# Optimization experiments

Hardware: AMD Instinct MI355X
Metric: run time of the kernel (lower is better)

The kernel has to match this reference:

```python
import jax, jax.numpy as jnp
import numpy as np

B, S, D_IN, M, H, F, L, D_OUT = 4, 1024, 256, 1024, 16, 8, 2, 256
HD = M // H
EPS = 1e-5


def setup_inputs() -> dict:
    key = jax.random.key(0)
    ks = iter(jax.random.split(key, 40))
    w = lambda *s: 0.02 * jax.random.normal(next(ks), s, dtype=jnp.float32)
    inp = {
        "x": jax.random.normal(next(ks), (B, S, D_IN), dtype=jnp.float32),
        # phase embedding params
        "Wemb": w(D_IN, M), "bemb": w(M),
        "Wamp": w(M, F), "bamp": w(F),
        "freqs": jnp.logspace(-1, 2, F, dtype=jnp.float32),
        "phase_off": w(F),
        # per-layer attention params, stacked on leading L axis
        "Wq": w(L, M, M), "bq": w(L, M),
        "Wk": w(L, M, M), "bk": w(L, M),
        "Wv": w(L, M, M), "bv": w(L, M),
        "Wo": w(L, M, M), "bo": w(L, M),
        "pbias": w(L, H, F),
        "ln_g": jnp.ones((L, M), dtype=jnp.float32),
        "ln_b": jnp.zeros((L, M), dtype=jnp.float32),
        # output projection MLP
        "W1": w(M, M // 2), "b1": w(M // 2),
        "W2": w(M // 2, D_OUT), "b2": w(D_OUT),
    }
    return inp


def _forward(x, Wemb, bemb, Wamp, bamp, freqs, phase_off,
             Wq, bq, Wk, bk, Wv, bv, Wo, bo, pbias, ln_g, ln_b,
             W1, b1, W2, b2):
    Bsz, Seq, _ = x.shape
    # --- TemporalPhaseEmbedding ---
    m = x @ Wemb + bemb                                   # [B,S,M]
    tc = jnp.arange(Seq, dtype=x.dtype) / Seq * (2.0 * jnp.pi)  # [S]
    amp = jax.nn.softmax(m @ Wamp + bamp, axis=-1)        # [B,S,F]
    pc = tc[:, None] * freqs[None, :] + phase_off         # [S,F] (batch-identical)
    # |m[...,None] * amp * e^{i*pc}| averaged over F == |m| * mean_F(amp)
    pf = jnp.abs(m) * jnp.mean(amp, axis=-1, keepdims=True)  # [B,S,M]
    # phase-coherence, batch-independent since pc is shared across batch
    coh = jnp.cos(pc[:, None, :] - pc[None, :, :])        # [S,S,F]
    scale = 1.0 / jnp.sqrt(jnp.asarray(HD, dtype=x.dtype))
    for l in range(L):
        res = pf
        Q = (pf @ Wq[l] + bq[l]).reshape(Bsz, Seq, H, HD)
        K = (pf @ Wk[l] + bk[l]).reshape(Bsz, Seq, H, HD)
        V = (pf @ Wv[l] + bv[l]).reshape(Bsz, Seq, H, HD)
        bias = jnp.einsum('stf,hf->hst', coh, pbias[l])   # [H,S,S]
        scores = jnp.einsum('bshd,bthd->bhst', Q, K) * scale + bias[None]
        w_attn = jax.nn.softmax(scores, axis=-1)
        att = jnp.einsum('bhst,bthd->bshd', w_attn, V).reshape(Bsz, Seq, M)
        att = att @ Wo[l] + bo[l]
        y = att + res
        mu = jnp.mean(y, axis=-1, keepdims=True)
        var = jnp.var(y, axis=-1, keepdims=True)
        pf = (y - mu) / jnp.sqrt(var + EPS) * ln_g[l] + ln_b[l]
    hdn = jax.nn.relu(pf @ W1 + b1)
    return hdn @ W2 + b2                                  # [B,S,D_OUT]


def reference(x, Wemb, bemb, Wamp, bamp, freqs, phase_off,
              Wq, bq, Wk, bk, Wv, bv, Wo, bo, pbias, ln_g, ln_b,
              W1, b1, W2, b2):
    return _forward(x, Wemb, bemb, Wamp, bamp, freqs, phase_off,
                    Wq, bq, Wk, bk, Wv, bv, Wo, bo, pbias, ln_g, ln_b,
                    W1, b1, W2, b2)
```

## Files before the change

kernel.cpp:

```cpp
#include <hip/hip_runtime.h>
#include <cmath>

#define B_    4
#define S_    1024
#define DIN_  256
#define M_    1024
#define H_    16
#define F_    8
#define L_    2
#define DOUT_ 256
#define NT_   4096

typedef unsigned short u16;
typedef unsigned int   u32;
typedef __bf16 bf16x8 __attribute__((ext_vector_type(8)));
typedef float  f32x4  __attribute__((ext_vector_type(4)));

#define LOG2E 1.4426950408889634f
#define QSCALE (0.125f * LOG2E)

__device__ __forceinline__ u16 f2b(float f) {
    u32 u = __builtin_bit_cast(u32, f);
    u += 0x7fffu + ((u >> 16) & 1u);
    return (u16)(u >> 16);
}
__device__ __forceinline__ float b2f(u32 h) {
    return __builtin_bit_cast(float, h << 16);
}
__device__ __forceinline__ void gload_lds16(const void* g, void* l) {
    __builtin_amdgcn_global_load_lds(
        (const __attribute__((address_space(1))) u32*)g,
        (__attribute__((address_space(3))) u32*)l, 16, 0, 0);
}

__global__ void qcsb_k(const float* __restrict__ freqs,
                       const float* __restrict__ poff,
                       const float* __restrict__ pb,
                       u16* __restrict__ qcs, u16* __restrict__ csb)
{
    const int QN = L_ * H_ * S_ * 16;
    int idx = blockIdx.x * 256 + threadIdx.x;
    if (idx < QN) {
        int f2 = idx & 15, f = f2 & 7;
        int s = (idx >> 4) & 1023;
        int lh = idx >> 14;
        float pc = ((float)s * (6.283185307179586f / 1024.f)) * freqs[f] + poff[f];
        float v = (f2 < 8) ? cosf(pc) : sinf(pc);
        qcs[idx] = f2b(pb[lh * 8 + f] * v * LOG2E);
    } else if (idx < QN + S_ * 16) {
        int i2 = idx - QN;
        int f2 = i2 & 15, f = f2 & 7;
        int s = i2 >> 4;
        float pc = ((float)s * (6.283185307179586f / 1024.f)) * freqs[f] + poff[f];
        csb[i2] = f2b((f2 < 8) ? cosf(pc) : sinf(pc));
    }
}

__global__ void bcat_k(const float* __restrict__ bq, const float* __restrict__ bk,
                       const float* __restrict__ bv, float* __restrict__ bqkv)
{
    int idx = blockIdx.x * 256 + threadIdx.x;
    int l = idx >= 3072;
    int j = idx - l * 3072;
    float v = (j < 1024) ? bq[l * 1024 + j]
            : (j < 2048) ? bk[l * 1024 + j - 1024]
                         : bv[l * 1024 + j - 2048];
    bqkv[idx] = v;
}

__global__ __launch_bounds__(256) void cvt_k(const float* __restrict__ src,
                                             u16* __restrict__ dst)
{
    int i = (blockIdx.x * 256 + threadIdx.x) * 4;
    float4 v = *(const float4*)(src + i);
    *(ushort4*)(dst + i) = make_ushort4(f2b(v.x), f2b(v.y), f2b(v.z), f2b(v.w));
}

__global__ __launch_bounds__(256) void cvtT_k(const float* __restrict__ src,
                                              u16* __restrict__ dst, int K, int N)
{
    __shared__ float t[32][33];
    src += (size_t)blockIdx.z * K * N;
    dst += (size_t)blockIdx.z * K * N;
    const int n0 = blockIdx.x * 32, k0 = blockIdx.y * 32;
    const int r = threadIdx.x >> 3, c4 = (threadIdx.x & 7) << 2;
    float4 v = *(const float4*)(src + (size_t)(k0 + r) * N + n0 + c4);
    t[r][c4 + 0] = v.x; t[r][c4 + 1] = v.y; t[r][c4 + 2] = v.z; t[r][c4 + 3] = v.w;
    __syncthreads();
    ushort4 o = make_ushort4(f2b(t[c4 + 0][r]), f2b(t[c4 + 1][r]),
                             f2b(t[c4 + 2][r]), f2b(t[c4 + 3][r]));
    *(ushort4*)(dst + (size_t)(n0 + r) * K + k0 + c4) = o;
}

__global__ __launch_bounds__(256) void cvtT3_k(const float* __restrict__ Wq,
                                               const float* __restrict__ Wk,
                                               const float* __restrict__ Wv,
                                               u16* __restrict__ dst)
{
    __shared__ float t[32][33];
    const int z = blockIdx.z, l = z / 3, which = z - l * 3;
    const float* src = (which == 0 ? Wq : which == 1 ? Wk : Wv) + (size_t)l * M_ * M_;
    u16* d = dst + (size_t)l * 3072 * 1024 + (size_t)which * 1024 * 1024;
    const int n0 = blockIdx.x * 32, k0 = blockIdx.y * 32;
    const int r = threadIdx.x >> 3, c4 = (threadIdx.x & 7) << 2;
    float4 v = *(const float4*)(src + (size_t)(k0 + r) * 1024 + n0 + c4);
    t[r][c4 + 0] = v.x; t[r][c4 + 1] = v.y; t[r][c4 + 2] = v.z; t[r][c4 + 3] = v.w;
    __syncthreads();
    ushort4 o = make_ushort4(f2b(t[c4 + 0][r]), f2b(t[c4 + 1][r]),
                             f2b(t[c4 + 2][r]), f2b(t[c4 + 3][r]));
    *(ushort4*)(d + (size_t)(n0 + r) * 1024 + k0 + c4) = o;
}

template<int EPI, int OUTBF>
__global__ __launch_bounds__(256, 2) void mgemm_k(
    const u16* __restrict__ A, const u16* __restrict__ Wt,
    const float* __restrict__ bias, void* __restrict__ Cout,
    u16* __restrict__ vt, int N, int K)
{
    __shared__ __attribute__((aligned(16))) u16 As[128 * 64];
    __shared__ __attribute__((aligned(16))) u16 Bs[128 * 64];
    const int tid = threadIdx.x;
    const int lane = tid & 63;
    const int bn = blockIdx.x, bm = blockIdx.y;
    const int wid = tid >> 6, wr = wid >> 1, wc = wid & 1;

    f32x4 acc[4][4];
#pragma unroll
    for (int m = 0; m < 4; ++m)
#pragma unroll
        for (int n = 0; n < 4; ++n) {
            f32x4 z = {0.f, 0.f, 0.f, 0.f};
            acc[m][n] = z;
        }

    const int r = lane & 15, g = lane >> 4;
    const int nk = K >> 6;

    for (int kt = 0; kt < nk; ++kt) {
        const int k0 = kt << 6;
        __syncthreads();
#pragma unroll
        for (int i = 0; i < 4; ++i) {
            int slot = i * 256 + tid;
            int row = slot >> 3;
            int kg = (slot & 7) ^ (row & 7);
            gload_lds16(A + (size_t)(bm * 128 + row) * K + k0 + kg * 8,
                        As + (size_t)(slot & ~63) * 8);
        }
#pragma unroll
        for (int i = 0; i < 4; ++i) {
            int slot = i * 256 + tid;
            int row = slot >> 3;
            int kg = (slot & 7) ^ (row & 7);
            gload_lds16(Wt + (size_t)(bn * 128 + row) * K + k0 + kg * 8,
                        Bs + (size_t)(slot & ~63) * 8);
        }
        __syncthreads();

#pragma unroll
        for (int ks = 0; ks < 2; ++ks) {
            bf16x8 af[4], bfr[4];
#pragma unroll
            for (int m = 0; m < 4; ++m) {
                int row = wr * 64 + m * 16 + r;
                int kg = (ks * 4 + g) ^ (row & 7);
                af[m] = *(const bf16x8*)(As + row * 64 + kg * 8);
            }
#pragma unroll
            for (int n = 0; n < 4; ++n) {
                int row = wc * 64 + n * 16 + r;
                int kg = (ks * 4 + g) ^ (row & 7);
                bfr[n] = *(const bf16x8*)(Bs + row * 64 + kg * 8);
            }
#pragma unroll
            for (int m = 0; m < 4; ++m)
#pragma unroll
                for (int n = 0; n < 4; ++n)
                    acc[m][n] = __builtin_amdgcn_mfma_f32_16x16x32_bf16(
                        af[m], bfr[n], acc[m][n], 0, 0, 0);
        }
    }

#pragma unroll
    for (int n = 0; n < 4; ++n) {
        const int gcol = bn * 128 + wc * 64 + n * 16 + r;
        const float bb = bias[gcol];
#pragma unroll
        for (int m = 0; m < 4; ++m) {
            const int grow0 = bm * 128 + wr * 64 + m * 16 + g * 4;
            if (EPI == 5 && gcol >= 2048) {
                int d = gcol - 2048;
                int bh = (grow0 >> 10) * 16 + (d >> 6);
                u16 pk[4];
#pragma unroll
                for (int q = 0; q < 4; ++q) pk[q] = f2b(acc[m][n][q] + bb);
                uint2 pv;
                pv.x = (u32)pk[0] | ((u32)pk[1] << 16);
                pv.y = (u32)pk[2] | ((u32)pk[3] << 16);
                *(uint2*)(vt + ((size_t)bh * 64 + (d & 63)) * 1024 + (grow0 & 1023)) = pv;
            } else {
#pragma unroll
                for (int q = 0; q < 4; ++q) {
                    float c = acc[m][n][q] + bb;
                    if (EPI == 1) c = fabsf(c) * 0.125f;
                    if (EPI == 2) c = fmaxf(c, 0.f);
                    if (EPI == 5) c = (gcol < 1024) ? c * QSCALE : c;
                    if (OUTBF)
                        ((u16*)Cout)[(size_t)(grow0 + q) * N + gcol] = f2b(c);
                    else
                        ((float*)Cout)[(size_t)(grow0 + q) * N + gcol] = c;
                }
            }
        }
    }
}

__global__ __launch_bounds__(512) void fattn_k(
    const u16* __restrict__ QKV, const u16* __restrict__ Vtg,
    const u16* __restrict__ csb, const u16* __restrict__ qcs,
    u16* __restrict__ Og)
{
    __shared__ __attribute__((aligned(16))) u16 Ks2[2][64 * 64];
    __shared__ __attribute__((aligned(16))) u16 Vt2[2][64 * 64];
    __shared__ __attribute__((aligned(16))) u16 Ext[2][64 * 16];
    __shared__ __attribute__((aligned(16))) u16 Pl[8][16 * 68];
    const int tid = threadIdx.x, lane = tid & 63, w = tid >> 6;
    const int c = lane & 15, g = lane >> 4;
    const int h = blockIdx.y, b = blockIdx.z, bh = b * 16 + h;
    const int s0 = blockIdx.x * 128;

    const uint4 zz = {0u, 0u, 0u, 0u};
    const bf16x8 zfrag = __builtin_bit_cast(bf16x8, zz);

    bf16x8 aq[3];
    {
        int sl = s0 + w * 16 + c;
        size_t tok = (size_t)b * 1024 + sl;
        aq[0] = *(const bf16x8*)(QKV + tok * 3072 + h * 64 + g * 8);
        aq[1] = *(const bf16x8*)(QKV + tok * 3072 + h * 64 + 32 + g * 8);
        aq[2] = (g < 2) ? *(const bf16x8*)(qcs + ((size_t)h * 1024 + sl) * 16 + g * 8)
                        : zfrag;
    }

    f32x4 oacc[4];
#pragma unroll
    for (int n = 0; n < 4; ++n) {
        f32x4 z = {0.f, 0.f, 0.f, 0.f};
        oacc[n] = z;
    }
    float lsum = 0.f;

    auto STAGE = [&](int buf, int t0) {
        int row = tid >> 3, gi = tid & 7;
        int kg = (gi ^ (row & 7)) * 8;
        gload_lds16(QKV + (size_t)(b * 1024 + t0 + row) * 3072 + 1024 + h * 64 + kg,
                    &Ks2[buf][(size_t)(tid & ~63) * 8]);
        gload_lds16(Vtg + (size_t)(bh * 64 + row) * 1024 + t0 + kg,
                    &Vt2[buf][(size_t)(tid & ~63) * 8]);
        if (tid < 128) {
            int r2 = tid >> 1, g2 = tid & 1;
            gload_lds16(csb + (size_t)(t0 + r2) * 16 + g2 * 8,
                        &Ext[buf][(size_t)(tid & ~63) * 8]);
        }
    };

    STAGE(0, 0);
    __builtin_amdgcn_sched_barrier(0);

    for (int it = 0; it < 16; ++it) {
        const int cur = it & 1;
        if (it < 15) {
            STAGE(cur ^ 1, (it + 1) << 6);
            if (w < 2) asm volatile("s_waitcnt vmcnt(3)" ::: "memory");
            else       asm volatile("s_waitcnt vmcnt(2)" ::: "memory");
        } else {
            asm volatile("s_waitcnt vmcnt(0)" ::: "memory");
        }
        __builtin_amdgcn_sched_barrier(0);
        __builtin_amdgcn_s_barrier();
        __builtin_amdgcn_sched_barrier(0);

        f32x4 sacc[4];
#pragma unroll
        for (int n = 0; n < 4; ++n) {
            f32x4 z = {0.f, 0.f, 0.f, 0.f};
            sacc[n] = z;
        }
        __builtin_amdgcn_s_setprio(1);
#pragma unroll
        for (int ks = 0; ks < 3; ++ks) {
            bf16x8 bk[4];
#pragma unroll
            for (int n = 0; n < 4; ++n) {
                int tr = n * 16 + c;
                if (ks < 2) {
                    int kg = (ks * 4 + g) ^ (tr & 7);
                    bk[n] = *(const bf16x8*)(&Ks2[cur][tr * 64 + kg * 8]);
                } else {
                    bk[n] = (g < 2) ? *(const bf16x8*)(&Ext[cur][tr * 16 + g * 8]) : zfrag;
                }
            }
#pragma unroll
            for (int n = 0; n < 4; ++n)
                sacc[n] = __builtin_amdgcn_mfma_f32_16x16x32_bf16(
                    bk[n], aq[ks], sacc[n], 0, 0, 0);
        }
        __builtin_amdgcn_s_setprio(0);

#pragma unroll
        for (int n = 0; n < 4; ++n) {
            u16 pk[4];
#pragma unroll
            for (int q = 0; q < 4; ++q) {
                float p = __builtin_amdgcn_exp2f(sacc[n][q]);
                lsum += p;
                pk[q] = f2b(p);
            }
            uint2 pv;
            pv.x = (u32)pk[0] | ((u32)pk[1] << 16);
            pv.y = (u32)pk[2] | ((u32)pk[3] << 16);
            *(uint2*)(&Pl[w][c * 68 + n * 16 + g * 4]) = pv;
        }

        __builtin_amdgcn_s_setprio(1);
#pragma unroll
        for (int ks2 = 0; ks2 < 2; ++ks2) {
            bf16x8 pa = *(const bf16x8*)(&Pl[w][c * 68 + ks2 * 32 + g * 8]);
#pragma unroll
            for (int n = 0; n < 4; ++n) {
                int dr = n * 16 + c;
                int kg = (ks2 * 4 + g) ^ (dr & 7);
                bf16x8 vf = *(const bf16x8*)(&Vt2[cur][dr * 64 + kg * 8]);
                oacc[n] = __builtin_amdgcn_mfma_f32_16x16x32_bf16(
                    pa, vf, oacc[n], 0, 0, 0);
            }
        }
        __builtin_amdgcn_s_setprio(0);

        __builtin_amdgcn_sched_barrier(0);
        __builtin_amdgcn_s_barrier();
        __builtin_amdgcn_sched_barrier(0);
    }

    float lt = lsum + __shfl_xor(lsum, 16);
    lt += __shfl_xor(lt, 32);
    float inv[4];
#pragma unroll
    for (int q = 0; q < 4; ++q)
        inv[q] = 1.f / __shfl(lt, g * 4 + q);

#pragma unroll
    for (int n = 0; n < 4; ++n)
#pragma unroll
        for (int q = 0; q < 4; ++q) {
            size_t tok = (size_t)b * 1024 + s0 + w * 16 + g * 4 + q;
            Og[tok * 1024 + h * 64 + n * 16 + c] = f2b(oacc[n][q] * inv[q]);
        }
}

__global__ __launch_bounds__(256) void ln_k(
    const u16* __restrict__ Y, u16* __restrict__ Pf,
    const float* __restrict__ g, const float* __restrict__ bt)
{
    const int rw = blockIdx.x;
    const int tid = threadIdx.x;
    const u16* yp = Y + (size_t)rw * M_ + tid * 4;
    u16* pp = Pf + (size_t)rw * M_ + tid * 4;
    ushort4 yv = *(const ushort4*)yp;
    ushort4 rv = *(const ushort4*)pp;
    float a[4];
    a[0] = b2f(yv.x) + b2f(rv.x); a[1] = b2f(yv.y) + b2f(rv.y);
    a[2] = b2f(yv.z) + b2f(rv.z); a[3] = b2f(yv.w) + b2f(rv.w);
    float s = a[0] + a[1] + a[2] + a[3];
    float q = a[0] * a[0] + a[1] * a[1] + a[2] * a[2] + a[3] * a[3];
#pragma unroll
    for (int o = 1; o < 64; o <<= 1) {
        s += __shfl_xor(s, o);
        q += __shfl_xor(q, o);
    }
    __shared__ float ss[4], qq[4];
    if ((tid & 63) == 0) { ss[tid >> 6] = s; qq[tid >> 6] = q; }
    __syncthreads();
    s = ss[0] + ss[1] + ss[2] + ss[3];
    q = qq[0] + qq[1] + qq[2] + qq[3];
    float mu = s * (1.0f / 1024.0f);
    float var = q * (1.0f / 1024.0f) - mu * mu;
    float inv = rsqrtf(var + 1e-5f);
    float4 gv = *(const float4*)(g + (tid << 2));
    float4 bv = *(const float4*)(bt + (tid << 2));
    *(ushort4*)pp = make_ushort4(
        f2b((a[0] - mu) * inv * gv.x + bv.x),
        f2b((a[1] - mu) * inv * gv.y + bv.y),
        f2b((a[2] - mu) * inv * gv.z + bv.z),
        f2b((a[3] - mu) * inv * gv.w + bv.w));
}

extern "C" void kernel_launch(void* const* d_in, const int* in_sizes, int n_in,
                              void* d_out, int out_size, void* d_ws, size_t ws_size,
                              hipStream_t stream)
{
    const float* x     = (const float*)d_in[0];
    const float* Wemb  = (const float*)d_in[1];
    const float* bemb  = (const float*)d_in[2];
    const float* freqs = (const float*)d_in[5];
    const float* poff  = (const float*)d_in[6];
    const float* Wq    = (const float*)d_in[7];
    const float* bq    = (const float*)d_in[8];
    const float* Wk    = (const float*)d_in[9];
    const float* bk    = (const float*)d_in[10];
    const float* Wv    = (const float*)d_in[11];
    const float* bv    = (const float*)d_in[12];
    const float* Wo    = (const float*)d_in[13];
    const float* bo    = (const float*)d_in[14];
    const float* pbias = (const float*)d_in[15];
    const float* lng   = (const float*)d_in[16];
    const float* lnb   = (const float*)d_in[17];
    const float* W1    = (const float*)d_in[18];
    const float* b1    = (const float*)d_in[19];
    const float* W2    = (const float*)d_in[20];
    const float* b2    = (const float*)d_in[21];
    float* out = (float*)d_out;

    char* ws = (char*)d_ws;
    const size_t MB = 1 << 20;
    u16* pf    = (u16*)(ws);
    u16* QKV   = (u16*)(ws + 8 * MB);
    u16* Ab    = (u16*)(ws + 32 * MB);
    u16* Vtg   = (u16*)(ws + 40 * MB);
    u16* WqkvT = (u16*)(ws + 48 * MB);
    u16* WoT   = (u16*)(ws + 60 * MB);
    u16* WembT = (u16*)(ws + 64 * MB);
    u16* W1T   = (u16*)(ws + 64 * MB + 512 * 1024);
    u16* W2T   = (u16*)(ws + 65 * MB + 512 * 1024);
    u16* xb    = (u16*)(ws + 66 * MB);
    u16* qcs   = (u16*)(ws + 68 * MB);
    u16* csb   = (u16*)(ws + 69 * MB);
    float* bqkv = (float*)(ws + 69 * MB + 64 * 1024);

    dim3 blk(256);
    cvt_k<<<1024, blk, 0, stream>>>(x, xb);
    cvtT3_k<<<dim3(32, 32, 6), blk, 0, stream>>>(Wq, Wk, Wv, WqkvT);
    cvtT_k<<<dim3(32, 32, 2), blk, 0, stream>>>(Wo, WoT, 1024, 1024);
    cvtT_k<<<dim3(32, 8, 1), blk, 0, stream>>>(Wemb, WembT, 256, 1024);
    cvtT_k<<<dim3(16, 32, 1), blk, 0, stream>>>(W1, W1T, 1024, 512);
    cvtT_k<<<dim3(8, 16, 1), blk, 0, stream>>>(W2, W2T, 512, 256);
    qcsb_k<<<2112, blk, 0, stream>>>(freqs, poff, pbias, qcs, csb);
    bcat_k<<<24, blk, 0, stream>>>(bq, bk, bv, bqkv);

    mgemm_k<1, 1><<<dim3(8, 32), blk, 0, stream>>>(xb, WembT, bemb, pf, nullptr, 1024, 256);

    for (int l = 0; l < L_; ++l) {
        mgemm_k<5, 1><<<dim3(24, 32), blk, 0, stream>>>(
            pf, WqkvT + (size_t)l * 3072 * 1024, bqkv + l * 3072, QKV, Vtg, 3072, 1024);
        fattn_k<<<dim3(8, 16, 4), dim3(512), 0, stream>>>(
            QKV, Vtg, csb, qcs + (size_t)l * H_ * S_ * 16, Ab);
        mgemm_k<0, 1><<<dim3(8, 32), blk, 0, stream>>>(
            Ab, WoT + (size_t)l * M_ * M_, bo + l * M_, QKV , nullptr, 1024, 1024);
        ln_k<<<dim3(NT_), blk, 0, stream>>>(QKV, pf, lng + l * M_, lnb + l * M_);
    }

    mgemm_k<2, 1><<<dim3(4, 32), blk, 0, stream>>>(pf, W1T, b1, Ab, nullptr, 512, 1024);
    mgemm_k<0, 0><<<dim3(2, 32), blk, 0, stream>>>(Ab, W2T, b2, out, nullptr, 256, 512);
}
```

Baseline: 259.5 us.

## Fuse prep kernels into one launch; attention waves handle two query tiles

Merges eight preprocessing kernels (casts, transposes, phase tables, bias concat) into one prep_k launch, dispatching on block index ranges to cut launch overhead. The attention kernel moves from 8 waves of 16 query rows to 4 waves of 32 rows each, so every K/V LDS fragment read feeds two MFMAs. The wait counts are adjusted for the doubled staging loads per thread. The cost is more accumulator registers per wave and fewer waves per block for hiding latency.

```diff
diff --git a/kernel.cpp b/kernel.cpp
--- a/kernel.cpp
+++ b/kernel.cpp
@@ -33,57 +33,11 @@
         (__attribute__((address_space(3))) u32*)l, 16, 0, 0);
 }
 
-__global__ void qcsb_k(const float* __restrict__ freqs,
-                       const float* __restrict__ poff,
-                       const float* __restrict__ pb,
-                       u16* __restrict__ qcs, u16* __restrict__ csb)
-{
-    const int QN = L_ * H_ * S_ * 16;
-    int idx = blockIdx.x * 256 + threadIdx.x;
-    if (idx < QN) {
-        int f2 = idx & 15, f = f2 & 7;
-        int s = (idx >> 4) & 1023;
-        int lh = idx >> 14;
-        float pc = ((float)s * (6.283185307179586f / 1024.f)) * freqs[f] + poff[f];
-        float v = (f2 < 8) ? cosf(pc) : sinf(pc);
-        qcs[idx] = f2b(pb[lh * 8 + f] * v * LOG2E);
-    } else if (idx < QN + S_ * 16) {
-        int i2 = idx - QN;
-        int f2 = i2 & 15, f = f2 & 7;
-        int s = i2 >> 4;
-        float pc = ((float)s * (6.283185307179586f / 1024.f)) * freqs[f] + poff[f];
-        csb[i2] = f2b((f2 < 8) ? cosf(pc) : sinf(pc));
-    }
-}
-
-__global__ void bcat_k(const float* __restrict__ bq, const float* __restrict__ bk,
-                       const float* __restrict__ bv, float* __restrict__ bqkv)
-{
-    int idx = blockIdx.x * 256 + threadIdx.x;
-    int l = idx >= 3072;
-    int j = idx - l * 3072;
-    float v = (j < 1024) ? bq[l * 1024 + j]
-            : (j < 2048) ? bk[l * 1024 + j - 1024]
-                         : bv[l * 1024 + j - 2048];
-    bqkv[idx] = v;
-}
-
-__global__ __launch_bounds__(256) void cvt_k(const float* __restrict__ src,
-                                             u16* __restrict__ dst)
-{
-    int i = (blockIdx.x * 256 + threadIdx.x) * 4;
-    float4 v = *(const float4*)(src + i);
-    *(ushort4*)(dst + i) = make_ushort4(f2b(v.x), f2b(v.y), f2b(v.z), f2b(v.w));
-}
-
-__global__ __launch_bounds__(256) void cvtT_k(const float* __restrict__ src,
-                                              u16* __restrict__ dst, int K, int N)
-{
-    __shared__ float t[32][33];
-    src += (size_t)blockIdx.z * K * N;
-    dst += (size_t)blockIdx.z * K * N;
-    const int n0 = blockIdx.x * 32, k0 = blockIdx.y * 32;
-    const int r = threadIdx.x >> 3, c4 = (threadIdx.x & 7) << 2;
+__device__ __forceinline__ void tileT(float (*t)[33], const float* src,
+                                      u16* dst, int K, int N, int n0, int k0,
+                                      int tid)
+{
+    const int r = tid >> 3, c4 = (tid & 7) << 2;
     float4 v = *(const float4*)(src + (size_t)(k0 + r) * N + n0 + c4);
     t[r][c4 + 0] = v.x; t[r][c4 + 1] = v.y; t[r][c4 + 2] = v.z; t[r][c4 + 3] = v.w;
     __syncthreads();
@@ -92,23 +46,77 @@
     *(ushort4*)(dst + (size_t)(n0 + r) * K + k0 + c4) = o;
 }
 
-__global__ __launch_bounds__(256) void cvtT3_k(const float* __restrict__ Wq,
-                                               const float* __restrict__ Wk,
-                                               const float* __restrict__ Wv,
-                                               u16* __restrict__ dst)
+__global__ __launch_bounds__(256) void prep_k(
+    const float* __restrict__ x, const float* __restrict__ Wemb,
+    const float* __restrict__ Wq, const float* __restrict__ Wk,
+    const float* __restrict__ Wv, const float* __restrict__ Wo,
+    const float* __restrict__ W1, const float* __restrict__ W2,
+    const float* __restrict__ freqs, const float* __restrict__ poff,
+    const float* __restrict__ pb, const float* __restrict__ bq,
+    const float* __restrict__ bk, const float* __restrict__ bv,
+    u16* __restrict__ xb, u16* __restrict__ WembT, u16* __restrict__ WqkvT,
+    u16* __restrict__ WoT, u16* __restrict__ W1T, u16* __restrict__ W2T,
+    u16* __restrict__ qcs, u16* __restrict__ csb, float* __restrict__ bqkv)
 {
     __shared__ float t[32][33];
-    const int z = blockIdx.z, l = z / 3, which = z - l * 3;
-    const float* src = (which == 0 ? Wq : which == 1 ? Wk : Wv) + (size_t)l * M_ * M_;
-    u16* d = dst + (size_t)l * 3072 * 1024 + (size_t)which * 1024 * 1024;
-    const int n0 = blockIdx.x * 32, k0 = blockIdx.y * 32;
-    const int r = threadIdx.x >> 3, c4 = (threadIdx.x & 7) << 2;
-    float4 v = *(const float4*)(src + (size_t)(k0 + r) * 1024 + n0 + c4);
-    t[r][c4 + 0] = v.x; t[r][c4 + 1] = v.y; t[r][c4 + 2] = v.z; t[r][c4 + 3] = v.w;
-    __syncthreads();
-    ushort4 o = make_ushort4(f2b(t[c4 + 0][r]), f2b(t[c4 + 1][r]),
-                             f2b(t[c4 + 2][r]), f2b(t[c4 + 3][r]));
-    *(ushort4*)(d + (size_t)(n0 + r) * 1024 + k0 + c4) = o;
+    const int bid = blockIdx.x, tid = threadIdx.x;
+
+    if (bid < 1024) {
+        int i = (bid * 256 + tid) * 4;
+        float4 v = *(const float4*)(x + i);
+        *(ushort4*)(xb + i) = make_ushort4(f2b(v.x), f2b(v.y), f2b(v.z), f2b(v.w));
+    } else if (bid < 7168) {
+        int id = bid - 1024;
+        int z = id >> 10, rem = id & 1023;
+        int n0 = (rem & 31) << 5, k0 = (rem >> 5) << 5;
+        int l = z / 3, which = z - l * 3;
+        const float* src = (which == 0 ? Wq : which == 1 ? Wk : Wv) + (size_t)l * M_ * M_;
+        u16* d = WqkvT + (size_t)l * 3072 * 1024 + (size_t)which * 1024 * 1024;
+        tileT(t, src, d, 1024, 1024, n0, k0, tid);
+    } else if (bid < 9216) {
+        int id = bid - 7168;
+        int z = id >> 10, rem = id & 1023;
+        int n0 = (rem & 31) << 5, k0 = (rem >> 5) << 5;
+        tileT(t, Wo + (size_t)z * M_ * M_, WoT + (size_t)z * M_ * M_,
+              1024, 1024, n0, k0, tid);
+    } else if (bid < 9472) {
+        int id = bid - 9216;
+        int n0 = (id & 31) << 5, k0 = (id >> 5) << 5;
+        tileT(t, Wemb, WembT, 256, 1024, n0, k0, tid);
+    } else if (bid < 9984) {
+        int id = bid - 9472;
+        int n0 = (id & 15) << 5, k0 = (id >> 4) << 5;
+        tileT(t, W1, W1T, 1024, 512, n0, k0, tid);
+    } else if (bid < 10112) {
+        int id = bid - 9984;
+        int n0 = (id & 7) << 5, k0 = (id >> 3) << 5;
+        tileT(t, W2, W2T, 512, 256, n0, k0, tid);
+    } else if (bid < 12224) {
+        const int QN = L_ * H_ * S_ * 16;
+        int idx = (bid - 10112) * 256 + tid;
+        if (idx < QN) {
+            int f2 = idx & 15, f = f2 & 7;
+            int s = (idx >> 4) & 1023;
+            int lh = idx >> 14;
+            float pc = ((float)s * (6.283185307179586f / 1024.f)) * freqs[f] + poff[f];
+            float v = (f2 < 8) ? cosf(pc) : sinf(pc);
+            qcs[idx] = f2b(pb[lh * 8 + f] * v * LOG2E);
+        } else {
+            int i2 = idx - QN;
+            int f2 = i2 & 15, f = f2 & 7;
+            int s = i2 >> 4;
+            float pc = ((float)s * (6.283185307179586f / 1024.f)) * freqs[f] + poff[f];
+            csb[i2] = f2b((f2 < 8) ? cosf(pc) : sinf(pc));
+        }
+    } else {
+        int idx = (bid - 12224) * 256 + tid;
+        int l = idx >= 3072;
+        int j = idx - l * 3072;
+        float v = (j < 1024) ? bq[l * 1024 + j]
+                : (j < 2048) ? bk[l * 1024 + j - 1024]
+                             : bv[l * 1024 + j - 2048];
+        bqkv[idx] = v;
+    }
 }
 
 template<int EPI, int OUTBF>
@@ -215,7 +223,7 @@
     }
 }
 
-__global__ __launch_bounds__(512) void fattn_k(
+__global__ __launch_bounds__(256) void fattn_k(
     const u16* __restrict__ QKV, const u16* __restrict__ Vtg,
     const u16* __restrict__ csb, const u16* __restrict__ qcs,
     u16* __restrict__ Og)
@@ -223,7 +231,7 @@
     __shared__ __attribute__((aligned(16))) u16 Ks2[2][64 * 64];
     __shared__ __attribute__((aligned(16))) u16 Vt2[2][64 * 64];
     __shared__ __attribute__((aligned(16))) u16 Ext[2][64 * 16];
-    __shared__ __attribute__((aligned(16))) u16 Pl[8][16 * 68];
+    __shared__ __attribute__((aligned(16))) u16 Pl[4][32 * 68];
     const int tid = threadIdx.x, lane = tid & 63, w = tid >> 6;
     const int c = lane & 15, g = lane >> 4;
     const int h = blockIdx.y, b = blockIdx.z, bh = b * 16 + h;
@@ -232,31 +240,38 @@
     const uint4 zz = {0u, 0u, 0u, 0u};
     const bf16x8 zfrag = __builtin_bit_cast(bf16x8, zz);
 
-    bf16x8 aq[3];
-    {
-        int sl = s0 + w * 16 + c;
+    bf16x8 aq[2][3];
+#pragma unroll
+    for (int m = 0; m < 2; ++m) {
+        int sl = s0 + w * 32 + m * 16 + c;
         size_t tok = (size_t)b * 1024 + sl;
-        aq[0] = *(const bf16x8*)(QKV + tok * 3072 + h * 64 + g * 8);
-        aq[1] = *(const bf16x8*)(QKV + tok * 3072 + h * 64 + 32 + g * 8);
-        aq[2] = (g < 2) ? *(const bf16x8*)(qcs + ((size_t)h * 1024 + sl) * 16 + g * 8)
-                        : zfrag;
-    }
-
-    f32x4 oacc[4];
-#pragma unroll
-    for (int n = 0; n < 4; ++n) {
-        f32x4 z = {0.f, 0.f, 0.f, 0.f};
-        oacc[n] = z;
-    }
-    float lsum = 0.f;
+        aq[m][0] = *(const bf16x8*)(QKV + tok * 3072 + h * 64 + g * 8);
+        aq[m][1] = *(const bf16x8*)(QKV + tok * 3072 + h * 64 + 32 + g * 8);
+        aq[m][2] = (g < 2) ? *(const bf16x8*)(qcs + ((size_t)h * 1024 + sl) * 16 + g * 8)
+                           : zfrag;
+    }
+
+    f32x4 oacc[2][4];
+#pragma unroll
+    for (int m = 0; m < 2; ++m)
+#pragma unroll
+        for (int n = 0; n < 4; ++n) {
+            f32x4 z = {0.f, 0.f, 0.f, 0.f};
+            oacc[m][n] = z;
+        }
+    float lsum[2] = {0.f, 0.f};
 
     auto STAGE = [&](int buf, int t0) {
-        int row = tid >> 3, gi = tid & 7;
-        int kg = (gi ^ (row & 7)) * 8;
-        gload_lds16(QKV + (size_t)(b * 1024 + t0 + row) * 3072 + 1024 + h * 64 + kg,
-                    &Ks2[buf][(size_t)(tid & ~63) * 8]);
-        gload_lds16(Vtg + (size_t)(bh * 64 + row) * 1024 + t0 + kg,
-                    &Vt2[buf][(size_t)(tid & ~63) * 8]);
+#pragma unroll
+        for (int i = 0; i < 2; ++i) {
+            int slot = i * 256 + tid;
+            int row = slot >> 3, gi = slot & 7;
+            int kg = (gi ^ (row & 7)) * 8;
+            gload_lds16(QKV + (size_t)(b * 1024 + t0 + row) * 3072 + 1024 + h * 64 + kg,
+                        &Ks2[buf][(size_t)(slot & ~63) * 8]);
+            gload_lds16(Vtg + (size_t)(bh * 64 + row) * 1024 + t0 + kg,
+                        &Vt2[buf][(size_t)(slot & ~63) * 8]);
+        }
         if (tid < 128) {
             int r2 = tid >> 1, g2 = tid & 1;
             gload_lds16(csb + (size_t)(t0 + r2) * 16 + g2 * 8,
@@ -271,8 +286,8 @@
         const int cur = it & 1;
         if (it < 15) {
             STAGE(cur ^ 1, (it + 1) << 6);
-            if (w < 2) asm volatile("s_waitcnt vmcnt(3)" ::: "memory");
-            else       asm volatile("s_waitcnt vmcnt(2)" ::: "memory");
+            if (w < 2) asm volatile("s_waitcnt vmcnt(5)" ::: "memory");
+            else       asm volatile("s_waitcnt vmcnt(4)" ::: "memory");
         } else {
             asm volatile("s_waitcnt vmcnt(0)" ::: "memory");
         }
@@ -280,12 +295,14 @@
         __builtin_amdgcn_s_barrier();
         __builtin_amdgcn_sched_barrier(0);
 
-        f32x4 sacc[4];
-#pragma unroll
-        for (int n = 0; n < 4; ++n) {
-            f32x4 z = {0.f, 0.f, 0.f, 0.f};
-            sacc[n] = z;
-        }
+        f32x4 sacc[2][4];
+#pragma unroll
+        for (int m = 0; m < 2; ++m)
+#pragma unroll
+            for (int n = 0; n < 4; ++n) {
+                f32x4 z = {0.f, 0.f, 0.f, 0.f};
+                sacc[m][n] = z;
+            }
         __builtin_amdgcn_s_setprio(1);
 #pragma unroll
         for (int ks = 0; ks < 3; ++ks) {
@@ -302,37 +319,46 @@
             }
 #pragma unroll
             for (int n = 0; n < 4; ++n)
-                sacc[n] = __builtin_amdgcn_mfma_f32_16x16x32_bf16(
-                    bk[n], aq[ks], sacc[n], 0, 0, 0);
+#pragma unroll
+                for (int m = 0; m < 2; ++m)
+                    sacc[m][n] = __builtin_amdgcn_mfma_f32_16x16x32_bf16(
+                        bk[n], aq[m][ks], sacc[m][n], 0, 0, 0);
         }
         __builtin_amdgcn_s_setprio(0);
 
 #pragma unroll
-        for (int n = 0; n < 4; ++n) {
-            u16 pk[4];
-#pragma unroll
-            for (int q = 0; q < 4; ++q) {
-                float p = __builtin_amdgcn_exp2f(sacc[n][q]);
-                lsum += p;
-                pk[q] = f2b(p);
-            }
-            uint2 pv;
-            pv.x = (u32)pk[0] | ((u32)pk[1] << 16);
-            pv.y = (u32)pk[2] | ((u32)pk[3] << 16);
-            *(uint2*)(&Pl[w][c * 68 + n * 16 + g * 4]) = pv;
-        }
+        for (int m = 0; m < 2; ++m)
+#pragma unroll
+            for (int n = 0; n < 4; ++n) {
+                u16 pk[4];
+#pragma unroll
+                for (int q = 0; q < 4; ++q) {
+                    float p = __builtin_amdgcn_exp2f(sacc[m][n][q]);
+                    lsum[m] += p;
+                    pk[q] = f2b(p);
+                }
+                uint2 pv;
+                pv.x = (u32)pk[0] | ((u32)pk[1] << 16);
+                pv.y = (u32)pk[2] | ((u32)pk[3] << 16);
+                *(uint2*)(&Pl[w][(m * 16 + c) * 68 + n * 16 + g * 4]) = pv;
+            }
 
         __builtin_amdgcn_s_setprio(1);
 #pragma unroll
         for (int ks2 = 0; ks2 < 2; ++ks2) {
-            bf16x8 pa = *(const bf16x8*)(&Pl[w][c * 68 + ks2 * 32 + g * 8]);
+            bf16x8 pa[2];
+#pragma unroll
+            for (int m = 0; m < 2; ++m)
+                pa[m] = *(const bf16x8*)(&Pl[w][(m * 16 + c) * 68 + ks2 * 32 + g * 8]);
 #pragma unroll
             for (int n = 0; n < 4; ++n) {
                 int dr = n * 16 + c;
                 int kg = (ks2 * 4 + g) ^ (dr & 7);
                 bf16x8 vf = *(const bf16x8*)(&Vt2[cur][dr * 64 + kg * 8]);
-                oacc[n] = __builtin_amdgcn_mfma_f32_16x16x32_bf16(
-                    pa, vf, oacc[n], 0, 0, 0);
+#pragma unroll
+                for (int m = 0; m < 2; ++m)
+                    oacc[m][n] = __builtin_amdgcn_mfma_f32_16x16x32_bf16(
+                        pa[m], vf, oacc[m][n], 0, 0, 0);
             }
         }
         __builtin_amdgcn_s_setprio(0);
@@ -342,20 +368,22 @@
         __builtin_amdgcn_sched_barrier(0);
     }
 
-    float lt = lsum + __shfl_xor(lsum, 16);
-    lt += __shfl_xor(lt, 32);
-    float inv[4];
-#pragma unroll
-    for (int q = 0; q < 4; ++q)
-        inv[q] = 1.f / __shfl(lt, g * 4 + q);
-
-#pragma unroll
-    for (int n = 0; n < 4; ++n)
-#pragma unroll
-        for (int q = 0; q < 4; ++q) {
-            size_t tok = (size_t)b * 1024 + s0 + w * 16 + g * 4 + q;
-            Og[tok * 1024 + h * 64 + n * 16 + c] = f2b(oacc[n][q] * inv[q]);
-        }
+#pragma unroll
+    for (int m = 0; m < 2; ++m) {
+        float lt = lsum[m] + __shfl_xor(lsum[m], 16);
+        lt += __shfl_xor(lt, 32);
+        float inv[4];
+#pragma unroll
+        for (int q = 0; q < 4; ++q)
+            inv[q] = 1.f / __shfl(lt, g * 4 + q);
+#pragma unroll
+        for (int n = 0; n < 4; ++n)
+#pragma unroll
+            for (int q = 0; q < 4; ++q) {
+                size_t tok = (size_t)b * 1024 + s0 + w * 32 + m * 16 + g * 4 + q;
+                Og[tok * 1024 + h * 64 + n * 16 + c] = f2b(oacc[m][n][q] * inv[q]);
+            }
+    }
 }
 
 __global__ __launch_bounds__(256) void ln_k(
@@ -438,21 +466,17 @@
     float* bqkv = (float*)(ws + 69 * MB + 64 * 1024);
 
     dim3 blk(256);
-    cvt_k<<<1024, blk, 0, stream>>>(x, xb);
-    cvtT3_k<<<dim3(32, 32, 6), blk, 0, stream>>>(Wq, Wk, Wv, WqkvT);
-    cvtT_k<<<dim3(32, 32, 2), blk, 0, stream>>>(Wo, WoT, 1024, 1024);
-    cvtT_k<<<dim3(32, 8, 1), blk, 0, stream>>>(Wemb, WembT, 256, 1024);
-    cvtT_k<<<dim3(16, 32, 1), blk, 0, stream>>>(W1, W1T, 1024, 512);
-    cvtT_k<<<dim3(8, 16, 1), blk, 0, stream>>>(W2, W2T, 512, 256);
-    qcsb_k<<<2112, blk, 0, stream>>>(freqs, poff, pbias, qcs, csb);
-    bcat_k<<<24, blk, 0, stream>>>(bq, bk, bv, bqkv);
+    prep_k<<<12248, blk, 0, stream>>>(x, Wemb, Wq, Wk, Wv, Wo, W1, W2,
+                                      freqs, poff, pbias, bq, bk, bv,
+                                      xb, WembT, WqkvT, WoT, W1T, W2T,
+                                      qcs, csb, bqkv);
 
     mgemm_k<1, 1><<<dim3(8, 32), blk, 0, stream>>>(xb, WembT, bemb, pf, nullptr, 1024, 256);
 
     for (int l = 0; l < L_; ++l) {
         mgemm_k<5, 1><<<dim3(24, 32), blk, 0, stream>>>(
             pf, WqkvT + (size_t)l * 3072 * 1024, bqkv + l * 3072, QKV, Vtg, 3072, 1024);
-        fattn_k<<<dim3(8, 16, 4), dim3(512), 0, stream>>>(
+        fattn_k<<<dim3(8, 16, 4), blk, 0, stream>>>(
             QKV, Vtg, csb, qcs + (size_t)l * H_ * S_ * 16, Ab);
         mgemm_k<0, 1><<<dim3(8, 32), blk, 0, stream>>>(
             Ab, WoT + (size_t)l * M_ * M_, bo + l * M_, QKV , nullptr, 1024, 1024);
```

Measured after the change: 252.4 us. 2.8% less time.
